# Optimization experiments

Hardware: AMD Instinct MI355X
Metric: run time of the kernel (lower is better)

The kernel has to match this reference:

```python
import jax, jax.numpy as jnp
import numpy as np

H, DK, DV, D, EPS = 4, 64, 64, 256, 1e-5

def setup_inputs() -> dict:
    key = jax.random.key(0)
    ks = jax.random.split(key, 12)
    B, L = 8, 2048
    s = 0.02
    return {
        "q": jax.random.normal(ks[0], (B, L, D), jnp.float32),
        "k": jax.random.normal(ks[1], (B, L, D), jnp.float32),
        "v": jax.random.normal(ks[2], (B, L, D), jnp.float32),
        "mask": jax.random.randint(ks[3], (B, L), 0, 2) > 0,
        "wq": s * jax.random.normal(ks[4], (D, H * DK), jnp.float32),
        "bq": jnp.zeros((H * DK,), jnp.float32),
        "wk": s * jax.random.normal(ks[5], (D, H * DK), jnp.float32),
        "bk": jnp.zeros((H * DK,), jnp.float32),
        "wv": s * jax.random.normal(ks[6], (D, H * DV), jnp.float32),
        "bv": jnp.zeros((H * DV,), jnp.float32),
        "wf": s * jax.random.normal(ks[7], (H * DV, D), jnp.float32),
        "bf": jnp.zeros((D,), jnp.float32),
        "gamma": jnp.ones((D,), jnp.float32),
        "beta": jnp.zeros((D,), jnp.float32),
    }

def reference(q, k, v, mask, wq, bq, wk, bk, wv, bv, wf, bf, gamma, beta):
    B, Lq, _ = q.shape
    Lk = k.shape[1]
    residual = q
    qh = (q @ wq + bq).reshape(B, Lq, H, DK)  # [B,L,H,dk]
    kh = (k @ wk + bk).reshape(B, Lk, H, DK)
    vh = (v @ wv + bv).reshape(B, Lk, H, DV)
    scores = jnp.einsum("bqhd,bkhd->bhqk", qh, kh) / jnp.sqrt(jnp.float32(DK))
    scores = jnp.where(mask[:, None, None, :], -jnp.inf, scores)
    attn = jax.nn.softmax(scores, axis=-1)  # [B,H,Lq,Lk]
    out = jnp.einsum("bhqk,bkhd->bqhd", attn, vh).reshape(B, Lq, H * DV)
    out = out @ wf + bf  # dropout is identity in eval mode
    x = out + residual
    mu = jnp.mean(x, axis=-1, keepdims=True)
    var = jnp.var(x, axis=-1, keepdims=True)
    out = gamma * (x - mu) * jax.lax.rsqrt(var + EPS) + beta
    # attn reshaped to torch layout (n_head*B, Lq, Lk)
    attn_t = attn.transpose(1, 0, 2, 3).reshape(H * B, Lq, Lk)
    return (out, attn_t)
```

## Files before the change

kernel.cpp:

```cpp
#include <hip/hip_runtime.h>
#include <hip/hip_bf16.h>

#define NH 4
#define DM 256
#define NB 8
#define NL 2048
#define LN_EPS 1e-5f

typedef __hip_bfloat16 bf16;
typedef __attribute__((ext_vector_type(8))) short short8;
typedef __attribute__((ext_vector_type(4))) short s16x4;
typedef __attribute__((ext_vector_type(4))) float f32x4;

#define MFMA(a, b, c) __builtin_amdgcn_mfma_f32_16x16x32_bf16((a), (b), (c), 0, 0, 0)

__device__ __forceinline__ short f2bf(float f) {
  __hip_bfloat16 h = __float2bfloat16(f);
  return *reinterpret_cast<short*>(&h);
}

__device__ __forceinline__ void gload16(const void* g, void* l) {
  __builtin_amdgcn_global_load_lds(
      (const __attribute__((address_space(1))) void*)g,
      (__attribute__((address_space(3))) void*)l, 16, 0, 0);
}

__device__ __forceinline__ int swz(int r, int cc) {
  return r * 128 + (((cc) ^ (r & 7)) << 4);
}

__global__ __launch_bounds__(256) void prep_kernel(
    const float* __restrict__ wq, const float* __restrict__ wk,
    const float* __restrict__ wv, const float* __restrict__ wf,
    const int* __restrict__ mask, bf16* __restrict__ wqT,
    bf16* __restrict__ wkT, bf16* __restrict__ wvT, bf16* __restrict__ wfT,
    float* __restrict__ maskadd) {
  int idx = blockIdx.x * 256 + threadIdx.x;
  if (idx < 4 * 65536) {
    int w = idx >> 16;
    int rem = idx & 65535;
    int k = rem >> 8, n = rem & 255;
    const float* src = (w == 0) ? wq : (w == 1) ? wk : (w == 2) ? wv : wf;
    bf16* dst = (w == 0) ? wqT : (w == 1) ? wkT : (w == 2) ? wvT : wfT;
    dst[n * 256 + k] = __float2bfloat16(src[k * 256 + n]);
  } else {
    int i = idx - 4 * 65536;
    if (i < NB * NL) maskadd[i] = mask[i] ? -1e30f : 0.0f;
  }
}

template <int MODE>
__global__ __launch_bounds__(256, 4) void proj_kernel(
    const float* __restrict__ x, const bf16* __restrict__ wT,
    const float* __restrict__ bias, float scale, bf16* __restrict__ out) {
  int lane = threadIdx.x & 63;
  int w = threadIdx.x >> 6;
  int col = lane & 15, g = lane >> 4;
  int rbase = blockIdx.x * 64 + w * 16;
  int cbase = blockIdx.y * 64;

  f32x4 acc[4] = {{0.f, 0.f, 0.f, 0.f},
                  {0.f, 0.f, 0.f, 0.f},
                  {0.f, 0.f, 0.f, 0.f},
                  {0.f, 0.f, 0.f, 0.f}};
  const float* ap = x + (size_t)(rbase + col) * DM;

#pragma unroll
  for (int ks = 0; ks < 8; ++ks) {
    int koff = ks * 32 + g * 8;
    f32x4 x0 = *(const f32x4*)(ap + koff);
    f32x4 x1 = *(const f32x4*)(ap + koff + 4);
    short8 a;
    a[0] = f2bf(x0[0]); a[1] = f2bf(x0[1]); a[2] = f2bf(x0[2]); a[3] = f2bf(x0[3]);
    a[4] = f2bf(x1[0]); a[5] = f2bf(x1[1]); a[6] = f2bf(x1[2]); a[7] = f2bf(x1[3]);
#pragma unroll
    for (int ct = 0; ct < 4; ++ct) {
      short8 b = *(const short8*)(wT + (size_t)(cbase + ct * 16 + col) * DM + koff);
      acc[ct] = MFMA(b, a, acc[ct]);
    }
  }

  int row = rbase + col;
  if (MODE == 0) {
    bf16* ob = out + (size_t)row * DM + cbase;
#pragma unroll
    for (int ct = 0; ct < 4; ++ct) {
      f32x4 bv = *(const f32x4*)(bias + cbase + ct * 16 + g * 4);
      s16x4 pk;
#pragma unroll
      for (int r = 0; r < 4; ++r) pk[r] = f2bf((acc[ct][r] + bv[r]) * scale);
      *(s16x4*)(ob + ct * 16 + g * 4) = pk;
    }
  } else {
    int bI = row >> 11, kpos = row & (NL - 1);
    int hh = cbase >> 6;
    bf16* obase = out + ((size_t)(bI * NH + hh) * 64) * NL + kpos;
#pragma unroll
    for (int ct = 0; ct < 4; ++ct) {
      f32x4 bv = *(const f32x4*)(bias + cbase + ct * 16 + g * 4);
#pragma unroll
      for (int r = 0; r < 4; ++r) {
        int dv = ct * 16 + g * 4 + r;
        obase[(size_t)dv * NL] = __float2bfloat16(acc[ct][r] + bv[r]);
      }
    }
  }
}

__global__ __launch_bounds__(256, 4) void attn_kernel(
    const bf16* __restrict__ qh, const bf16* __restrict__ kh,
    const bf16* __restrict__ vhT, const float* __restrict__ maskadd,
    float* __restrict__ attn_f, float* __restrict__ aout) {
  __shared__ char lds[40960];

  int lane = threadIdx.x & 63;
  int w = threadIdx.x >> 6;
  int col = lane & 15, g = lane >> 4;
  char* pb = lds + 32768 + w * 2048;

  int bid = blockIdx.x;
  int qt = bid & 31;
  int bh = bid >> 5;
  int b = bh & 7, h = bh >> 3;
  int qbase = qt * 64 + w * 16;

  const bf16* qrow = qh + (size_t)(b * NL + qbase + col) * DM + h * 64;
  short8 aq0 = *(const short8*)(qrow + g * 8);
  short8 aq1 = *(const short8*)(qrow + 32 + g * 8);

  const bf16* khb = kh + (size_t)(b * NL) * DM + h * 64;
  const bf16* vtb = vhT + (size_t)((b * NH + h) * 64) * NL;
  const float* madd_b = maskadd + b * NL;

  int srow = lane >> 3;
  int scol = ((lane & 7) ^ srow) * 8;
  int ldsw = w * 1024;

  char* kcur = lds;
  char* knxt = lds + 8192;
  char* vcur = lds + 16384;
  char* vnxt = lds + 24576;

#pragma unroll
  for (int rr = 0; rr < 2; ++rr)
    gload16(khb + (size_t)(rr * 32 + w * 8 + srow) * DM + scol,
            kcur + rr * 4096 + ldsw);
  __syncthreads();

  float l = 0.f;
  for (int kt = 0; kt < NL; kt += 64) {
    if (kt + 64 < NL) {
#pragma unroll
      for (int rr = 0; rr < 2; ++rr)
        gload16(khb + (size_t)(kt + 64 + rr * 32 + w * 8 + srow) * DM + scol,
                knxt + rr * 4096 + ldsw);
    }
#pragma unroll
    for (int ct = 0; ct < 4; ++ct) {
      int r = ct * 16 + col;
      short8 b0 = *(const short8*)(kcur + swz(r, g));
      short8 b1 = *(const short8*)(kcur + swz(r, g + 4));
      f32x4 c = {0.f, 0.f, 0.f, 0.f};
      c = MFMA(b0, aq0, c);
      c = MFMA(b1, aq1, c);
      f32x4 ma = *(const f32x4*)(madd_b + kt + ct * 16 + g * 4);
      l += __expf(c[0] + ma[0]) + __expf(c[1] + ma[1]) +
           __expf(c[2] + ma[2]) + __expf(c[3] + ma[3]);
    }
    __syncthreads();
    char* t = kcur; kcur = knxt; knxt = t;
  }
  l += __shfl_xor(l, 16);
  l += __shfl_xor(l, 32);
  float inv_l = 1.0f / l;

  f32x4 accO[4] = {{0.f, 0.f, 0.f, 0.f},
                   {0.f, 0.f, 0.f, 0.f},
                   {0.f, 0.f, 0.f, 0.f},
                   {0.f, 0.f, 0.f, 0.f}};
  float* attn_base = attn_f + (size_t)bh * NL * NL + (size_t)(qbase + col) * NL;

#pragma unroll
  for (int rr = 0; rr < 2; ++rr) {
    gload16(khb + (size_t)(rr * 32 + w * 8 + srow) * DM + scol,
            kcur + rr * 4096 + ldsw);
    gload16(vtb + (size_t)(rr * 32 + w * 8 + srow) * NL + scol,
            vcur + rr * 4096 + ldsw);
  }
  __syncthreads();

  for (int kt = 0; kt < NL; kt += 64) {
    if (kt + 64 < NL) {
#pragma unroll
      for (int rr = 0; rr < 2; ++rr) {
        gload16(khb + (size_t)(kt + 64 + rr * 32 + w * 8 + srow) * DM + scol,
                knxt + rr * 4096 + ldsw);
        gload16(vtb + (size_t)(rr * 32 + w * 8 + srow) * NL + (kt + 64) + scol,
                vnxt + rr * 4096 + ldsw);
      }
    }
#pragma unroll
    for (int ct = 0; ct < 4; ++ct) {
      int r = ct * 16 + col;
      short8 b0 = *(const short8*)(kcur + swz(r, g));
      short8 b1 = *(const short8*)(kcur + swz(r, g + 4));
      f32x4 c = {0.f, 0.f, 0.f, 0.f};
      c = MFMA(b0, aq0, c);
      c = MFMA(b1, aq1, c);
      f32x4 ma = *(const f32x4*)(madd_b + kt + ct * 16 + g * 4);
      f32x4 p;
      p[0] = __expf(c[0] + ma[0]) * inv_l;
      p[1] = __expf(c[1] + ma[1]) * inv_l;
      p[2] = __expf(c[2] + ma[2]) * inv_l;
      p[3] = __expf(c[3] + ma[3]) * inv_l;
      *(f32x4*)(attn_base + kt + ct * 16 + g * 4) = p;
      s16x4 pk;
      pk[0] = f2bf(p[0]); pk[1] = f2bf(p[1]);
      pk[2] = f2bf(p[2]); pk[3] = f2bf(p[3]);
      *(s16x4*)(pb + col * 128 + ((ct * 32 + g * 8) ^ ((col & 7) << 4))) = pk;
    }
    short8 ap0 = *(const short8*)(pb + swz(col, g));
    short8 ap1 = *(const short8*)(pb + swz(col, g + 4));
#pragma unroll
    for (int dvt = 0; dvt < 4; ++dvt) {
      int r = dvt * 16 + col;
      short8 v0 = *(const short8*)(vcur + swz(r, g));
      short8 v1 = *(const short8*)(vcur + swz(r, g + 4));
      accO[dvt] = MFMA(ap0, v0, accO[dvt]);
      accO[dvt] = MFMA(ap1, v1, accO[dvt]);
    }
    __syncthreads();
    char* t = kcur; kcur = knxt; knxt = t;
    t = vcur; vcur = vnxt; vnxt = t;
  }

#pragma unroll
  for (int dvt = 0; dvt < 4; ++dvt)
#pragma unroll
    for (int r = 0; r < 4; ++r)
      aout[(size_t)(b * NL + qbase + g * 4 + r) * DM + h * 64 + dvt * 16 + col] =
          accO[dvt][r];
}

__global__ __launch_bounds__(256, 4) void final_kernel(
    const float* __restrict__ aout, const bf16* __restrict__ wfT,
    const float* __restrict__ bf_, const float* __restrict__ resid,
    const float* __restrict__ gamma, const float* __restrict__ beta,
    float* __restrict__ out) {
  __shared__ float lsum[16][4];
  __shared__ float lsq[16][4];
  int lane = threadIdx.x & 63;
  int w = threadIdx.x >> 6;
  int col = lane & 15, g = lane >> 4;
  int rbase = blockIdx.x * 16;

  f32x4 acc[4];
#pragma unroll
  for (int ct = 0; ct < 4; ++ct) acc[ct] = (f32x4){0.f, 0.f, 0.f, 0.f};

  const float* ap = aout + (size_t)(rbase + col) * DM;
#pragma unroll
  for (int ks = 0; ks < 8; ++ks) {
    int koff = ks * 32 + g * 8;
    f32x4 x0 = *(const f32x4*)(ap + koff);
    f32x4 x1 = *(const f32x4*)(ap + koff + 4);
    short8 a;
    a[0] = f2bf(x0[0]); a[1] = f2bf(x0[1]); a[2] = f2bf(x0[2]); a[3] = f2bf(x0[3]);
    a[4] = f2bf(x1[0]); a[5] = f2bf(x1[1]); a[6] = f2bf(x1[2]); a[7] = f2bf(x1[3]);
#pragma unroll
    for (int ct = 0; ct < 4; ++ct) {
      short8 b = *(const short8*)(wfT + (size_t)(w * 64 + ct * 16 + col) * DM + koff);
      acc[ct] = MFMA(b, a, acc[ct]);
    }
  }

  int row = rbase + col;
  float sum = 0.f, sq = 0.f;
#pragma unroll
  for (int ct = 0; ct < 4; ++ct) {
    f32x4 bv = *(const f32x4*)(bf_ + w * 64 + ct * 16 + g * 4);
    f32x4 rs = *(const f32x4*)(resid + (size_t)row * DM + w * 64 + ct * 16 + g * 4);
#pragma unroll
    for (int r = 0; r < 4; ++r) {
      float xv = acc[ct][r] + bv[r] + rs[r];
      acc[ct][r] = xv;
      sum += xv;
      sq += xv * xv;
    }
  }
  sum += __shfl_xor(sum, 16); sum += __shfl_xor(sum, 32);
  sq += __shfl_xor(sq, 16);  sq += __shfl_xor(sq, 32);
  if (lane < 16) {
    lsum[col][w] = sum;
    lsq[col][w] = sq;
  }
  __syncthreads();
  float s_ = lsum[col][0] + lsum[col][1] + lsum[col][2] + lsum[col][3];
  float q_ = lsq[col][0] + lsq[col][1] + lsq[col][2] + lsq[col][3];
  float mu = s_ * (1.0f / 256.0f);
  float var = q_ * (1.0f / 256.0f) - mu * mu;
  float rstd = rsqrtf(var + LN_EPS);
#pragma unroll
  for (int ct = 0; ct < 4; ++ct) {
    f32x4 gm = *(const f32x4*)(gamma + w * 64 + ct * 16 + g * 4);
    f32x4 bt = *(const f32x4*)(beta + w * 64 + ct * 16 + g * 4);
    f32x4 o;
#pragma unroll
    for (int r = 0; r < 4; ++r)
      o[r] = gm[r] * (acc[ct][r] - mu) * rstd + bt[r];
    *(f32x4*)(out + (size_t)row * DM + w * 64 + ct * 16 + g * 4) = o;
  }
}

extern "C" void kernel_launch(void* const* d_in, const int* in_sizes, int n_in,
                              void* d_out, int out_size, void* d_ws,
                              size_t ws_size, hipStream_t stream) {
  const float* q     = (const float*)d_in[0];
  const float* k     = (const float*)d_in[1];
  const float* v     = (const float*)d_in[2];
  const int*   mask  = (const int*)d_in[3];
  const float* wq    = (const float*)d_in[4];
  const float* bq    = (const float*)d_in[5];
  const float* wk    = (const float*)d_in[6];
  const float* bk    = (const float*)d_in[7];
  const float* wv    = (const float*)d_in[8];
  const float* bv    = (const float*)d_in[9];
  const float* wf    = (const float*)d_in[10];
  const float* bf_   = (const float*)d_in[11];
  const float* gamma = (const float*)d_in[12];
  const float* beta  = (const float*)d_in[13];

  char* ws = (char*)d_ws;
  bf16* wqT = (bf16*)(ws);
  bf16* wkT = (bf16*)(ws + (1 << 17));
  bf16* wvT = (bf16*)(ws + 2 * (1 << 17));
  bf16* wfT = (bf16*)(ws + 3 * (1 << 17));
  float* maskadd = (float*)(ws + 4 * (1 << 17));
  bf16* qh = (bf16*)(ws + 4 * (1 << 17) + (1 << 16));
  bf16* kh = qh + (size_t)16384 * 256;
  bf16* vhT = kh + (size_t)16384 * 256;
  float* aout = (float*)(vhT + (size_t)16384 * 256);

  float* out_f = (float*)d_out;
  float* attn_f = out_f + (size_t)16384 * 256;

  prep_kernel<<<1088, 256, 0, stream>>>(wq, wk, wv, wf, mask, wqT, wkT, wvT,
                                        wfT, maskadd);
  proj_kernel<0><<<dim3(256, 4), 256, 0, stream>>>(q, wqT, bq, 0.125f, qh);
  proj_kernel<0><<<dim3(256, 4), 256, 0, stream>>>(k, wkT, bk, 1.0f, kh);
  proj_kernel<1><<<dim3(256, 4), 256, 0, stream>>>(v, wvT, bv, 1.0f, vhT);
  attn_kernel<<<1024, 256, 0, stream>>>(qh, kh, vhT, maskadd, attn_f, aout);
  final_kernel<<<1024, 256, 0, stream>>>(aout, wfT, bf_, q, gamma, beta, out_f);
}
```

Baseline: 783.1 us.

## Load K/V directly into registers, remap attention blocks, merge QKV projections

The attention kernel stops staging K and V tiles through double-buffered LDS with async global-to-LDS loads and barriers. Each wave now reads its K and V fragments straight from global memory into registers, which cuts LDS use to the small P buffer and removes the per-tile __syncthreads. Block indices are remapped so that consecutive workgroups spread across batch/head groups, likely to suit the multi-XCD L2 layout. The three projection launches are also merged into one launch over a z grid dimension. The cost is that each wave now loads K/V redundantly from global or L2, with less latency hiding.

Measured after the change: 1.035 ms. 32.2% more time.

```diff
diff --git a/kernel.cpp b/kernel.cpp
--- a/kernel.cpp
+++ b/kernel.cpp
@@ -17,12 +17,6 @@
 __device__ __forceinline__ short f2bf(float f) {
   __hip_bfloat16 h = __float2bfloat16(f);
   return *reinterpret_cast<short*>(&h);
-}
-
-__device__ __forceinline__ void gload16(const void* g, void* l) {
-  __builtin_amdgcn_global_load_lds(
-      (const __attribute__((address_space(1))) void*)g,
-      (__attribute__((address_space(3))) void*)l, 16, 0, 0);
 }
 
 __device__ __forceinline__ int swz(int r, int cc) {
@@ -49,10 +43,19 @@
   }
 }
 
-template <int MODE>
 __global__ __launch_bounds__(256, 4) void proj_kernel(
-    const float* __restrict__ x, const bf16* __restrict__ wT,
-    const float* __restrict__ bias, float scale, bf16* __restrict__ out) {
+    const float* __restrict__ qx, const float* __restrict__ kx,
+    const float* __restrict__ vx, const bf16* __restrict__ wqT,
+    const bf16* __restrict__ wkT, const bf16* __restrict__ wvT,
+    const float* __restrict__ bq, const float* __restrict__ bk,
+    const float* __restrict__ bv, bf16* __restrict__ qh,
+    bf16* __restrict__ kh, bf16* __restrict__ vhT) {
+  int z = blockIdx.z;
+  const float* x = (z == 0) ? qx : (z == 1) ? kx : vx;
+  const bf16* wT = (z == 0) ? wqT : (z == 1) ? wkT : wvT;
+  const float* bias = (z == 0) ? bq : (z == 1) ? bk : bv;
+  float scale = (z == 0) ? 0.125f : 1.0f;
+
   int lane = threadIdx.x & 63;
   int w = threadIdx.x >> 6;
   int col = lane & 15, g = lane >> 4;
@@ -81,27 +84,27 @@
   }
 
   int row = rbase + col;
-  if (MODE == 0) {
-    bf16* ob = out + (size_t)row * DM + cbase;
-#pragma unroll
-    for (int ct = 0; ct < 4; ++ct) {
-      f32x4 bv = *(const f32x4*)(bias + cbase + ct * 16 + g * 4);
+  if (z < 2) {
+    bf16* ob = ((z == 0) ? qh : kh) + (size_t)row * DM + cbase;
+#pragma unroll
+    for (int ct = 0; ct < 4; ++ct) {
+      f32x4 bvv = *(const f32x4*)(bias + cbase + ct * 16 + g * 4);
       s16x4 pk;
 #pragma unroll
-      for (int r = 0; r < 4; ++r) pk[r] = f2bf((acc[ct][r] + bv[r]) * scale);
+      for (int r = 0; r < 4; ++r) pk[r] = f2bf((acc[ct][r] + bvv[r]) * scale);
       *(s16x4*)(ob + ct * 16 + g * 4) = pk;
     }
   } else {
     int bI = row >> 11, kpos = row & (NL - 1);
     int hh = cbase >> 6;
-    bf16* obase = out + ((size_t)(bI * NH + hh) * 64) * NL + kpos;
-#pragma unroll
-    for (int ct = 0; ct < 4; ++ct) {
-      f32x4 bv = *(const f32x4*)(bias + cbase + ct * 16 + g * 4);
+    bf16* obase = vhT + ((size_t)(bI * NH + hh) * 64) * NL + kpos;
+#pragma unroll
+    for (int ct = 0; ct < 4; ++ct) {
+      f32x4 bvv = *(const f32x4*)(bias + cbase + ct * 16 + g * 4);
 #pragma unroll
       for (int r = 0; r < 4; ++r) {
         int dv = ct * 16 + g * 4 + r;
-        obase[(size_t)dv * NL] = __float2bfloat16(acc[ct][r] + bv[r]);
+        obase[(size_t)dv * NL] = __float2bfloat16(acc[ct][r] + bvv[r]);
       }
     }
   }
@@ -111,14 +114,15 @@
     const bf16* __restrict__ qh, const bf16* __restrict__ kh,
     const bf16* __restrict__ vhT, const float* __restrict__ maskadd,
     float* __restrict__ attn_f, float* __restrict__ aout) {
-  __shared__ char lds[40960];
+  __shared__ char lds[8192];
 
   int lane = threadIdx.x & 63;
   int w = threadIdx.x >> 6;
   int col = lane & 15, g = lane >> 4;
-  char* pb = lds + 32768 + w * 2048;
-
-  int bid = blockIdx.x;
+  char* pb = lds + w * 2048;
+
+  int wg = blockIdx.x;
+  int bid = ((wg & 7) << 7) | (wg >> 3);
   int qt = bid & 31;
   int bh = bid >> 5;
   int b = bh & 7, h = bh >> 3;
@@ -132,43 +136,24 @@
   const bf16* vtb = vhT + (size_t)((b * NH + h) * 64) * NL;
   const float* madd_b = maskadd + b * NL;
 
-  int srow = lane >> 3;
-  int scol = ((lane & 7) ^ srow) * 8;
-  int ldsw = w * 1024;
-
-  char* kcur = lds;
-  char* knxt = lds + 8192;
-  char* vcur = lds + 16384;
-  char* vnxt = lds + 24576;
-
-#pragma unroll
-  for (int rr = 0; rr < 2; ++rr)
-    gload16(khb + (size_t)(rr * 32 + w * 8 + srow) * DM + scol,
-            kcur + rr * 4096 + ldsw);
-  __syncthreads();
-
   float l = 0.f;
   for (int kt = 0; kt < NL; kt += 64) {
-    if (kt + 64 < NL) {
-#pragma unroll
-      for (int rr = 0; rr < 2; ++rr)
-        gload16(khb + (size_t)(kt + 64 + rr * 32 + w * 8 + srow) * DM + scol,
-                knxt + rr * 4096 + ldsw);
-    }
-#pragma unroll
-    for (int ct = 0; ct < 4; ++ct) {
-      int r = ct * 16 + col;
-      short8 b0 = *(const short8*)(kcur + swz(r, g));
-      short8 b1 = *(const short8*)(kcur + swz(r, g + 4));
+    short8 kb[8];
+#pragma unroll
+    for (int ct = 0; ct < 4; ++ct) {
+      const bf16* kpr = khb + (size_t)(kt + ct * 16 + col) * DM;
+      kb[2 * ct] = *(const short8*)(kpr + g * 8);
+      kb[2 * ct + 1] = *(const short8*)(kpr + 32 + g * 8);
+    }
+#pragma unroll
+    for (int ct = 0; ct < 4; ++ct) {
       f32x4 c = {0.f, 0.f, 0.f, 0.f};
-      c = MFMA(b0, aq0, c);
-      c = MFMA(b1, aq1, c);
+      c = MFMA(kb[2 * ct], aq0, c);
+      c = MFMA(kb[2 * ct + 1], aq1, c);
       f32x4 ma = *(const f32x4*)(madd_b + kt + ct * 16 + g * 4);
       l += __expf(c[0] + ma[0]) + __expf(c[1] + ma[1]) +
            __expf(c[2] + ma[2]) + __expf(c[3] + ma[3]);
     }
-    __syncthreads();
-    char* t = kcur; kcur = knxt; knxt = t;
   }
   l += __shfl_xor(l, 16);
   l += __shfl_xor(l, 32);
@@ -180,33 +165,19 @@
                    {0.f, 0.f, 0.f, 0.f}};
   float* attn_base = attn_f + (size_t)bh * NL * NL + (size_t)(qbase + col) * NL;
 
-#pragma unroll
-  for (int rr = 0; rr < 2; ++rr) {
-    gload16(khb + (size_t)(rr * 32 + w * 8 + srow) * DM + scol,
-            kcur + rr * 4096 + ldsw);
-    gload16(vtb + (size_t)(rr * 32 + w * 8 + srow) * NL + scol,
-            vcur + rr * 4096 + ldsw);
-  }
-  __syncthreads();
-
   for (int kt = 0; kt < NL; kt += 64) {
-    if (kt + 64 < NL) {
-#pragma unroll
-      for (int rr = 0; rr < 2; ++rr) {
-        gload16(khb + (size_t)(kt + 64 + rr * 32 + w * 8 + srow) * DM + scol,
-                knxt + rr * 4096 + ldsw);
-        gload16(vtb + (size_t)(rr * 32 + w * 8 + srow) * NL + (kt + 64) + scol,
-                vnxt + rr * 4096 + ldsw);
-      }
-    }
-#pragma unroll
-    for (int ct = 0; ct < 4; ++ct) {
-      int r = ct * 16 + col;
-      short8 b0 = *(const short8*)(kcur + swz(r, g));
-      short8 b1 = *(const short8*)(kcur + swz(r, g + 4));
+    short8 kb[8];
+#pragma unroll
+    for (int ct = 0; ct < 4; ++ct) {
+      const bf16* kpr = khb + (size_t)(kt + ct * 16 + col) * DM;
+      kb[2 * ct] = *(const short8*)(kpr + g * 8);
+      kb[2 * ct + 1] = *(const short8*)(kpr + 32 + g * 8);
+    }
+#pragma unroll
+    for (int ct = 0; ct < 4; ++ct) {
       f32x4 c = {0.f, 0.f, 0.f, 0.f};
-      c = MFMA(b0, aq0, c);
-      c = MFMA(b1, aq1, c);
+      c = MFMA(kb[2 * ct], aq0, c);
+      c = MFMA(kb[2 * ct + 1], aq1, c);
       f32x4 ma = *(const f32x4*)(madd_b + kt + ct * 16 + g * 4);
       f32x4 p;
       p[0] = __expf(c[0] + ma[0]) * inv_l;
@@ -219,19 +190,20 @@
       pk[2] = f2bf(p[2]); pk[3] = f2bf(p[3]);
       *(s16x4*)(pb + col * 128 + ((ct * 32 + g * 8) ^ ((col & 7) << 4))) = pk;
     }
+    short8 vb[8];
+#pragma unroll
+    for (int dvt = 0; dvt < 4; ++dvt) {
+      const bf16* vp = vtb + (size_t)(dvt * 16 + col) * NL + kt;
+      vb[2 * dvt] = *(const short8*)(vp + g * 8);
+      vb[2 * dvt + 1] = *(const short8*)(vp + 32 + g * 8);
+    }
     short8 ap0 = *(const short8*)(pb + swz(col, g));
     short8 ap1 = *(const short8*)(pb + swz(col, g + 4));
 #pragma unroll
     for (int dvt = 0; dvt < 4; ++dvt) {
-      int r = dvt * 16 + col;
-      short8 v0 = *(const short8*)(vcur + swz(r, g));
-      short8 v1 = *(const short8*)(vcur + swz(r, g + 4));
-      accO[dvt] = MFMA(ap0, v0, accO[dvt]);
-      accO[dvt] = MFMA(ap1, v1, accO[dvt]);
-    }
-    __syncthreads();
-    char* t = kcur; kcur = knxt; knxt = t;
-    t = vcur; vcur = vnxt; vnxt = t;
+      accO[dvt] = MFMA(ap0, vb[2 * dvt], accO[dvt]);
+      accO[dvt] = MFMA(ap1, vb[2 * dvt + 1], accO[dvt]);
+    }
   }
 
 #pragma unroll
@@ -346,9 +318,8 @@
 
   prep_kernel<<<1088, 256, 0, stream>>>(wq, wk, wv, wf, mask, wqT, wkT, wvT,
                                         wfT, maskadd);
-  proj_kernel<0><<<dim3(256, 4), 256, 0, stream>>>(q, wqT, bq, 0.125f, qh);
-  proj_kernel<0><<<dim3(256, 4), 256, 0, stream>>>(k, wkT, bk, 1.0f, kh);
-  proj_kernel<1><<<dim3(256, 4), 256, 0, stream>>>(v, wvT, bv, 1.0f, vhT);
+  proj_kernel<<<dim3(256, 4, 3), 256, 0, stream>>>(q, k, v, wqT, wkT, wvT, bq,
+                                                   bk, bv, qh, kh, vhT);
   attn_kernel<<<1024, 256, 0, stream>>>(qh, kh, vhT, maskadd, attn_f, aout);
   final_kernel<<<1024, 256, 0, stream>>>(aout, wfT, bf_, q, gamma, beta, out_f);
 }
```
